# Optimization experiments

Measured on AMD Instinct MI355X. Metric: run time of the kernel, lower is better.

## Reference

```python
import jax, jax.numpy as jnp
import numpy as np


def _make_constraint_mask(n=9):
    N = n * n
    rows = np.arange(N) // n
    cols = np.arange(N) % n
    box = (rows // 3) * 3 + cols // 3
    cm = np.stack([
        rows[:, None] == rows[None, :],
        cols[:, None] == cols[None, :],
        box[:, None] == box[None, :],
    ], axis=1).astype(np.float32)  # (N, 3, N)
    return cm


def setup_inputs() -> dict:
    n, H, B = 9, 100, 512
    N = n * n
    key = jax.random.key(0)
    k1, k2, k3, k4 = jax.random.split(key, 4)
    digits = jax.random.randint(k1, (B, N), 0, n)
    keep = jax.random.bernoulli(k2, 0.5, (B, N)).astype(jnp.float32)
    x = jax.nn.one_hot(digits, n, dtype=jnp.float32) * keep[..., None]
    constraint_mask = jnp.asarray(_make_constraint_mask(n))  # (81, 3, 81)
    W1 = jax.random.normal(k3, (H, 3 * n), jnp.float32) / np.sqrt(3 * n).astype(np.float32)
    W2 = jax.random.normal(k4, (n, H), jnp.float32) / np.sqrt(H).astype(np.float32)
    return {"x": x, "constraint_mask": constraint_mask, "W1": W1, "W2": W2}


def reference(x, constraint_mask, W1, W2):
    B, N, n = x.shape
    bidx = jnp.arange(B)

    def step(carry, _):
        x, x_pred = carry
        # sparse constraint aggregation: constraints[b,i,k,v] = sum_j cm[i,k,j] * x[b,j,v]
        constraints = jnp.einsum('ikj,bjv->bikv', constraint_mask, x)  # (B,N,3,n)
        empty = x.sum(-1) == 0  # (B,N) cells still unfilled
        f = constraints.reshape(B, N, 3 * n)
        s_ = jax.nn.softmax(jax.nn.relu(f @ W1.T) @ W2.T, axis=-1)  # (B,N,n)
        x_pred = jnp.where(empty[..., None], s_, x_pred)
        s = jnp.where(empty[..., None], s_, 0.0)
        score = s.max(-1)          # (B,N)
        pos = s.argmax(-1)         # (B,N) best digit per cell
        mmax = jnp.argmax(score, axis=1)  # (B,) most confident cell
        has_empty = empty.any(axis=1)     # rows with remaining empties get a write
        p = pos[bidx, mmax]
        old = x[bidx, mmax, p]
        x = x.at[bidx, mmax, p].set(jnp.where(has_empty, 1.0, old))
        return (x, x_pred), None

    # Original loops min_empty (= max empties in batch) times; iterations past a
    # row's fill point are exact no-ops, so a fixed N=n*n steps gives identical output.
    (x, x_pred), _ = jax.lax.scan(step, (x, x), None, length=N)
    return (x_pred, x)
```

## Files before the change

kernel.cpp:

```cpp
#include <hip/hip_runtime.h>
#include <math.h>


#define NCELL 81
#define ND 9
#define NH 100
#define NG 27
#define NTHREADS 256

__global__ __launch_bounds__(NTHREADS, 2)
void sudoku_solver_kernel(const float* __restrict__ x_in,
                          const float* __restrict__ W1,
                          const float* __restrict__ W2,
                          float* __restrict__ out,
                          int B)
{
    __shared__ float xs[NCELL * ND];
    __shared__ float xp[NCELL * ND];
    __shared__ float gsum[NG * ND];
    alignas(16) __shared__ float PT[NG * NH];
    __shared__ float escore[NCELL];
    __shared__ int   epos[NCELL];
    __shared__ int   elist[NCELL];
    __shared__ int   wlist[NCELL];
    __shared__ int   EcntS, Wcnt;

    const int b   = blockIdx.x;
    const int tid = threadIdx.x;
    if (b >= B) return;

    const int lane = tid & 63;
    const int wv   = tid >> 6;
    const int sgrp = lane / 9;
    const int vd   = lane - 9 * sgrp;
    const int u    = tid % NH;
    const int sub  = tid / NH;

    float w1r[NG];
    if (tid < 2 * NH) {
        #pragma unroll
        for (int k = 0; k < NG; ++k) w1r[k] = W1[u * NG + k];
    }
    float4 w2r[25];
    {
        const float4* w2row = (const float4*)&W2[vd * NH];
        #pragma unroll
        for (int q = 0; q < 25; ++q) w2r[q] = w2row[q];
    }

    {
        const float* xb = x_in + (size_t)b * (NCELL * ND);
        for (int i = tid; i < NCELL * ND; i += NTHREADS) {
            float v = xb[i];
            xs[i] = v;
            xp[i] = v;
        }
    }
    if (tid == 0) EcntS = 0;
    __syncthreads();

    for (int t = tid; t < NCELL + NG * ND; t += NTHREADS) {
        if (t < NCELL) {
            const float* r = &xs[t * ND];
            float s = r[0]+r[1]+r[2]+r[3]+r[4]+r[5]+r[6]+r[7]+r[8];
            if (s == 0.0f) { int e = atomicAdd(&EcntS, 1); elist[e] = t; }
        } else {
            int g = (t - NCELL) / ND;
            int v = (t - NCELL) % ND;
            float acc = 0.0f;
            if (g < 9) {
                int base = g * 9;
                #pragma unroll
                for (int j = 0; j < 9; ++j) acc += xs[(base + j) * ND + v];
            } else if (g < 18) {
                int c = g - 9;
                #pragma unroll
                for (int j = 0; j < 9; ++j) acc += xs[(j * 9 + c) * ND + v];
            } else {
                int bb = g - 18;
                int br = (bb / 3) * 3, bc2 = (bb % 3) * 3;
                #pragma unroll
                for (int j = 0; j < 9; ++j)
                    acc += xs[((br + j / 3) * 9 + (bc2 + j % 3)) * ND + v];
            }
            gsum[g * ND + v] = acc;
        }
    }
    __syncthreads();

    int E_reg = EcntS;
    if (tid < 2 * NH) {
        for (int g = sub; g < NG; g += 2) {
            const float* gv = &gsum[g * ND];
            float acc = 0.0f;
            if (g < 9) {
                #pragma unroll
                for (int v = 0; v < ND; ++v) acc = fmaf(w1r[v],      gv[v], acc);
            } else if (g < 18) {
                #pragma unroll
                for (int v = 0; v < ND; ++v) acc = fmaf(w1r[9 + v],  gv[v], acc);
            } else {
                #pragma unroll
                for (int v = 0; v < ND; ++v) acc = fmaf(w1r[18 + v], gv[v], acc);
            }
            PT[g * NH + u] = acc;
        }
    }
    for (int i = tid; i < E_reg; i += NTHREADS) wlist[i] = elist[i];
    __syncthreads();

    int W_reg = E_reg;
    int pend_cell = -1, pend_digit = 0, pend_be = 0;

    while (E_reg > 0) {
        if (tid == 63) {
            Wcnt = 0;
            if (pend_cell >= 0) {
                int fr = pend_cell / 9, fc = pend_cell % 9;
                int fb = (fr / 3) * 3 + fc / 3;
                xs[pend_cell * ND + pend_digit] = 1.0f;
                gsum[fr * ND + pend_digit]        += 1.0f;
                gsum[(9 + fc) * ND + pend_digit]  += 1.0f;
                gsum[(18 + fb) * ND + pend_digit] += 1.0f;
                elist[pend_be] = elist[E_reg];
            }
        }
        const int npass = (W_reg + 27) / 28;
        for (int pass = 0; pass < npass; ++pass) {
            int ci = pass * 28 + wv * 7 + sgrp;
            if (sgrp < 7 && ci < W_reg) {
                int cell = wlist[ci];
                int r = cell / 9, c = cell - 9 * r;
                int bg = 18 + (r / 3) * 3 + c / 3;
                const float4* p_r = (const float4*)&PT[r * NH];
                const float4* p_c = (const float4*)&PT[(9 + c) * NH];
                const float4* p_b = (const float4*)&PT[bg * NH];
                float a0 = 0.0f, a1 = 0.0f;
                #pragma unroll
                for (int q = 0; q < 25; ++q) {
                    float4 hr = p_r[q], hc = p_c[q], hb = p_b[q];
                    float hx = fmaxf((hr.x + hc.x) + hb.x, 0.0f);
                    float hy = fmaxf((hr.y + hc.y) + hb.y, 0.0f);
                    float hz = fmaxf((hr.z + hc.z) + hb.z, 0.0f);
                    float hw = fmaxf((hr.w + hc.w) + hb.w, 0.0f);
                    float4 w = w2r[q];
                    a0 = fmaf(w.x, hx, a0);
                    a0 = fmaf(w.y, hy, a0);
                    a1 = fmaf(w.z, hz, a1);
                    a1 = fmaf(w.w, hw, a1);
                }
                float l_own = a0 + a1;
                float l[9];
                #pragma unroll
                for (int j = 0; j < 9; ++j) l[j] = __shfl(l_own, 9 * sgrp + j, 64);
                float m = -INFINITY;
                #pragma unroll
                for (int j = 0; j < 9; ++j) m = fmaxf(m, l[j]);
                float e9[9]; float ss = 0.0f;
                #pragma unroll
                for (int j = 0; j < 9; ++j) { e9[j] = expf(l[j] - m); ss += e9[j]; }
                float best = -1.0f; int bp = 0; float svown = 0.0f;
                #pragma unroll
                for (int j = 0; j < 9; ++j) {
                    float sv = e9[j] / ss;
                    if (j == vd) svown = sv;
                    if (sv > best) { best = sv; bp = j; }
                }
                xp[cell * ND + vd] = svown;
                if (vd == 0) { escore[cell] = best; epos[cell] = bp; }
            }
        }
        __syncthreads();

        float bs = -1.0f; int bc = 0x7fffffff, bp = 0, be = 0;
        for (int e = lane; e < E_reg; e += 64) {
            int ce = elist[e];
            float sc = escore[ce];
            if (sc > bs || (sc == bs && ce < bc)) { bs = sc; bc = ce; bp = epos[ce]; be = e; }
        }
        #pragma unroll
        for (int off = 32; off > 0; off >>= 1) {
            float os = __shfl_xor(bs, off, 64);
            int   oc = __shfl_xor(bc, off, 64);
            int   op = __shfl_xor(bp, off, 64);
            int   oe = __shfl_xor(be, off, 64);
            if (os > bs || (os == bs && oc < bc)) { bs = os; bc = oc; bp = op; be = oe; }
        }
        const int fr = bc / 9, fc = bc % 9, fb = (fr / 3) * 3 + fc / 3;

        int Wn = 0;
        for (int base = 0; base < E_reg; base += 64) {
            int e = base + lane;
            bool pr = false;
            int ce = 0;
            if (e < E_reg && e != be) {
                ce = elist[e];
                int r = ce / 9, c = ce - 9 * r;
                pr = (r == fr) || (c == fc) || (((r / 3) * 3 + c / 3) == fb);
            }
            unsigned long long mask = __ballot(pr);
            Wn += (int)__popcll(mask);
            if (wv == 0 && pr) { int w = atomicAdd(&Wcnt, 1); wlist[w] = ce; }
        }

        if (tid < 2 * NH) {
            if (sub == 0) {
                const float* gv = &gsum[fr * ND];
                float acc = 0.0f;
                #pragma unroll
                for (int v = 0; v < ND; ++v) {
                    float g = gv[v] + ((v == bp) ? 1.0f : 0.0f);
                    acc = fmaf(w1r[v], g, acc);
                }
                PT[fr * NH + u] = acc;
                const float* gv2 = &gsum[(18 + fb) * ND];
                float acc2 = 0.0f;
                #pragma unroll
                for (int v = 0; v < ND; ++v) {
                    float g = gv2[v] + ((v == bp) ? 1.0f : 0.0f);
                    acc2 = fmaf(w1r[18 + v], g, acc2);
                }
                PT[(18 + fb) * NH + u] = acc2;
            } else {
                const float* gv = &gsum[(9 + fc) * ND];
                float acc = 0.0f;
                #pragma unroll
                for (int v = 0; v < ND; ++v) {
                    float g = gv[v] + ((v == bp) ? 1.0f : 0.0f);
                    acc = fmaf(w1r[9 + v], g, acc);
                }
                PT[(9 + fc) * NH + u] = acc;
            }
        }

        E_reg -= 1;
        pend_cell = bc; pend_digit = bp; pend_be = be;
        W_reg = Wn;
        __syncthreads();
    }

    if (tid == 63 && pend_cell >= 0) xs[pend_cell * ND + pend_digit] = 1.0f;
    __syncthreads();

    const size_t outb = (size_t)b * (NCELL * ND);
    const size_t half = (size_t)B * (NCELL * ND);
    for (int i = tid; i < NCELL * ND; i += NTHREADS) {
        out[outb + i]        = xp[i];
        out[half + outb + i] = xs[i];
    }
}

extern "C" void kernel_launch(void* const* d_in, const int* in_sizes, int n_in,
                              void* d_out, int out_size, void* d_ws, size_t ws_size,
                              hipStream_t stream)
{
    const float* x  = (const float*)d_in[0];
    const float* W1 = (const float*)d_in[2];
    const float* W2 = (const float*)d_in[3];
    float* out = (float*)d_out;
    const int B = in_sizes[0] / (NCELL * ND);

    sudoku_solver_kernel<<<dim3(B), dim3(NTHREADS), 0, stream>>>(x, W1, W2, out, B);
}
```

Before: 249.5 us.

## Precompute hidden activations across all threads and pack argmax into single 64-bit key

Adds a pre-pass in which all 256 threads compute the ReLU hidden vectors for every cell needing refresh into a new shared buffer, so the per-cell dot-product loop only reads one vector instead of three. The pass costs an extra block-wide barrier per iteration and adds about 32KB of shared memory, which may lower occupancy. Packs score, cell and index into one 64-bit key so the wave reduction needs a single shuffle per step. Pads gsum rows to 12 floats so they can be read with float4 loads.

```diff
diff --git a/kernel.cpp b/kernel.cpp
--- a/kernel.cpp
+++ b/kernel.cpp
@@ -6,7 +6,25 @@
 #define ND 9
 #define NH 100
 #define NG 27
+#define GP 12
 #define NTHREADS 256
+
+template<int OFF>
+__device__ __forceinline__ float pt_dot(const float* __restrict__ gr,
+                                        const float (&w1r)[NG], int bp)
+{
+    float g[9];
+    float4 ga = *(const float4*)gr;
+    float4 gb = *(const float4*)(gr + 4);
+    g[0]=ga.x; g[1]=ga.y; g[2]=ga.z; g[3]=ga.w;
+    g[4]=gb.x; g[5]=gb.y; g[6]=gb.z; g[7]=gb.w;
+    g[8]=gr[8];
+    float acc = 0.0f;
+    #pragma unroll
+    for (int v = 0; v < 9; ++v)
+        acc = fmaf(w1r[OFF + v], g[v] + ((v == bp) ? 1.0f : 0.0f), acc);
+    return acc;
+}
 
 __global__ __launch_bounds__(NTHREADS, 2)
 void sudoku_solver_kernel(const float* __restrict__ x_in,
@@ -17,8 +35,9 @@
 {
     __shared__ float xs[NCELL * ND];
     __shared__ float xp[NCELL * ND];
-    __shared__ float gsum[NG * ND];
+    alignas(16) __shared__ float gsum[NG * GP];
     alignas(16) __shared__ float PT[NG * NH];
+    alignas(16) __shared__ float hs[NCELL * NH];
     __shared__ float escore[NCELL];
     __shared__ int   epos[NCELL];
     __shared__ int   elist[NCELL];
@@ -83,7 +102,7 @@
                 for (int j = 0; j < 9; ++j)
                     acc += xs[((br + j / 3) * 9 + (bc2 + j % 3)) * ND + v];
             }
-            gsum[g * ND + v] = acc;
+            gsum[g * GP + v] = acc;
         }
     }
     __syncthreads();
@@ -91,18 +110,10 @@
     int E_reg = EcntS;
     if (tid < 2 * NH) {
         for (int g = sub; g < NG; g += 2) {
-            const float* gv = &gsum[g * ND];
-            float acc = 0.0f;
-            if (g < 9) {
-                #pragma unroll
-                for (int v = 0; v < ND; ++v) acc = fmaf(w1r[v],      gv[v], acc);
-            } else if (g < 18) {
-                #pragma unroll
-                for (int v = 0; v < ND; ++v) acc = fmaf(w1r[9 + v],  gv[v], acc);
-            } else {
-                #pragma unroll
-                for (int v = 0; v < ND; ++v) acc = fmaf(w1r[18 + v], gv[v], acc);
-            }
+            float acc;
+            if (g < 9)       acc = pt_dot<0>(&gsum[g * GP], w1r, -1);
+            else if (g < 18) acc = pt_dot<9>(&gsum[g * GP], w1r, -1);
+            else             acc = pt_dot<18>(&gsum[g * GP], w1r, -1);
             PT[g * NH + u] = acc;
         }
     }
@@ -113,41 +124,49 @@
     int pend_cell = -1, pend_digit = 0, pend_be = 0;
 
     while (E_reg > 0) {
-        if (tid == 63) {
+        if (tid == NTHREADS - 1) {
             Wcnt = 0;
             if (pend_cell >= 0) {
                 int fr = pend_cell / 9, fc = pend_cell % 9;
                 int fb = (fr / 3) * 3 + fc / 3;
                 xs[pend_cell * ND + pend_digit] = 1.0f;
-                gsum[fr * ND + pend_digit]        += 1.0f;
-                gsum[(9 + fc) * ND + pend_digit]  += 1.0f;
-                gsum[(18 + fb) * ND + pend_digit] += 1.0f;
+                gsum[fr * GP + pend_digit]        += 1.0f;
+                gsum[(9 + fc) * GP + pend_digit]  += 1.0f;
+                gsum[(18 + fb) * GP + pend_digit] += 1.0f;
                 elist[pend_be] = elist[E_reg];
             }
         }
+        for (int ch = tid; ch < W_reg * 25; ch += NTHREADS) {
+            int wi = ch / 25, qc = ch - 25 * wi;
+            int cell = wlist[wi];
+            int r = cell / 9, c = cell - 9 * r;
+            int bg = 18 + (r / 3) * 3 + c / 3;
+            float4 hr = ((const float4*)&PT[r * NH])[qc];
+            float4 hc = ((const float4*)&PT[(9 + c) * NH])[qc];
+            float4 hb = ((const float4*)&PT[bg * NH])[qc];
+            float4 h;
+            h.x = fmaxf((hr.x + hc.x) + hb.x, 0.0f);
+            h.y = fmaxf((hr.y + hc.y) + hb.y, 0.0f);
+            h.z = fmaxf((hr.z + hc.z) + hb.z, 0.0f);
+            h.w = fmaxf((hr.w + hc.w) + hb.w, 0.0f);
+            ((float4*)&hs[wi * NH])[qc] = h;
+        }
+        __syncthreads();
+
         const int npass = (W_reg + 27) / 28;
         for (int pass = 0; pass < npass; ++pass) {
             int ci = pass * 28 + wv * 7 + sgrp;
             if (sgrp < 7 && ci < W_reg) {
                 int cell = wlist[ci];
-                int r = cell / 9, c = cell - 9 * r;
-                int bg = 18 + (r / 3) * 3 + c / 3;
-                const float4* p_r = (const float4*)&PT[r * NH];
-                const float4* p_c = (const float4*)&PT[(9 + c) * NH];
-                const float4* p_b = (const float4*)&PT[bg * NH];
+                const float4* h4 = (const float4*)&hs[ci * NH];
                 float a0 = 0.0f, a1 = 0.0f;
                 #pragma unroll
                 for (int q = 0; q < 25; ++q) {
-                    float4 hr = p_r[q], hc = p_c[q], hb = p_b[q];
-                    float hx = fmaxf((hr.x + hc.x) + hb.x, 0.0f);
-                    float hy = fmaxf((hr.y + hc.y) + hb.y, 0.0f);
-                    float hz = fmaxf((hr.z + hc.z) + hb.z, 0.0f);
-                    float hw = fmaxf((hr.w + hc.w) + hb.w, 0.0f);
-                    float4 w = w2r[q];
-                    a0 = fmaf(w.x, hx, a0);
-                    a0 = fmaf(w.y, hy, a0);
-                    a1 = fmaf(w.z, hz, a1);
-                    a1 = fmaf(w.w, hw, a1);
+                    float4 hv = h4[q], w = w2r[q];
+                    a0 = fmaf(w.x, hv.x, a0);
+                    a0 = fmaf(w.y, hv.y, a0);
+                    a1 = fmaf(w.z, hv.z, a1);
+                    a1 = fmaf(w.w, hv.w, a1);
                 }
                 float l_own = a0 + a1;
                 float l[9];
@@ -172,20 +191,24 @@
         }
         __syncthreads();
 
-        float bs = -1.0f; int bc = 0x7fffffff, bp = 0, be = 0;
+        unsigned long long key = 0ULL;
         for (int e = lane; e < E_reg; e += 64) {
             int ce = elist[e];
             float sc = escore[ce];
-            if (sc > bs || (sc == bs && ce < bc)) { bs = sc; bc = ce; bp = epos[ce]; be = e; }
+            unsigned int lo = ((unsigned)(NCELL - ce) << 7) | (unsigned)e;
+            unsigned long long k =
+                ((unsigned long long)__float_as_uint(sc) << 32) | lo;
+            if (k > key) key = k;
         }
         #pragma unroll
         for (int off = 32; off > 0; off >>= 1) {
-            float os = __shfl_xor(bs, off, 64);
-            int   oc = __shfl_xor(bc, off, 64);
-            int   op = __shfl_xor(bp, off, 64);
-            int   oe = __shfl_xor(be, off, 64);
-            if (os > bs || (os == bs && oc < bc)) { bs = os; bc = oc; bp = op; be = oe; }
-        }
+            unsigned long long ok = __shfl_xor(key, off, 64);
+            if (ok > key) key = ok;
+        }
+        const unsigned int lo = (unsigned int)key;
+        const int bc = NCELL - (int)(lo >> 7);
+        const int be = (int)(lo & 127);
+        const int bp = epos[bc];
         const int fr = bc / 9, fc = bc % 9, fb = (fr / 3) * 3 + fc / 3;
 
         int Wn = 0;
@@ -205,31 +228,10 @@
 
         if (tid < 2 * NH) {
             if (sub == 0) {
-                const float* gv = &gsum[fr * ND];
-                float acc = 0.0f;
-                #pragma unroll
-                for (int v = 0; v < ND; ++v) {
-                    float g = gv[v] + ((v == bp) ? 1.0f : 0.0f);
-                    acc = fmaf(w1r[v], g, acc);
-                }
-                PT[fr * NH + u] = acc;
-                const float* gv2 = &gsum[(18 + fb) * ND];
-                float acc2 = 0.0f;
-                #pragma unroll
-                for (int v = 0; v < ND; ++v) {
-                    float g = gv2[v] + ((v == bp) ? 1.0f : 0.0f);
-                    acc2 = fmaf(w1r[18 + v], g, acc2);
-                }
-                PT[(18 + fb) * NH + u] = acc2;
+                PT[fr * NH + u]        = pt_dot<0>(&gsum[fr * GP], w1r, bp);
+                PT[(18 + fb) * NH + u] = pt_dot<18>(&gsum[(18 + fb) * GP], w1r, bp);
             } else {
-                const float* gv = &gsum[(9 + fc) * ND];
-                float acc = 0.0f;
-                #pragma unroll
-                for (int v = 0; v < ND; ++v) {
-                    float g = gv[v] + ((v == bp) ? 1.0f : 0.0f);
-                    acc = fmaf(w1r[9 + v], g, acc);
-                }
-                PT[(9 + fc) * NH + u] = acc;
+                PT[(9 + fc) * NH + u]  = pt_dot<9>(&gsum[(9 + fc) * GP], w1r, bp);
             }
         }
 
@@ -239,7 +241,8 @@
         __syncthreads();
     }
 
-    if (tid == 63 && pend_cell >= 0) xs[pend_cell * ND + pend_digit] = 1.0f;
+    if (tid == NTHREADS - 1 && pend_cell >= 0)
+        xs[pend_cell * ND + pend_digit] = 1.0f;
     __syncthreads();
 
     const size_t outb = (size_t)b * (NCELL * ND);
```

Result: faster. 206.6 us (-17.2%).
